# Kernel tuning notes

Measured on AMD Instinct MI355X. Metric: run time of the kernel, lower is better.

Reference implementation:

```python
import jax, jax.numpy as jnp
import numpy as np
import math

B, S = 8, 2048
N_HIDDEN_RNN = 512
D_MODEL = 1024
NUM_HEADS = 16
N_OUTPUT = 1024
SCALE = math.sqrt(D_MODEL // NUM_HEADS)  # head_dim used only for scaling


def setup_inputs() -> dict:
    key = jax.random.key(0)
    ks = jax.random.split(key, 11)
    def lin(k, fan_in, fan_out):
        bound = 1.0 / math.sqrt(fan_in)
        kw, kb = jax.random.split(k)
        W = jax.random.uniform(kw, (fan_out, fan_in), jnp.float32, -bound, bound)
        b = jax.random.uniform(kb, (fan_out,), jnp.float32, -bound, bound)
        return W, b
    Wq, bq = lin(ks[0], N_HIDDEN_RNN, D_MODEL)
    Wk, bk = lin(ks[1], D_MODEL, D_MODEL)
    Wv, bv = lin(ks[2], D_MODEL, D_MODEL)
    Wo, bo = lin(ks[3], D_MODEL, N_OUTPUT)
    return {
        "query": jax.random.normal(ks[4], (B, S, N_HIDDEN_RNN), jnp.float32),
        "key": jax.random.normal(ks[5], (B, S, D_MODEL), jnp.float32),
        "value": jax.random.normal(ks[6], (B, S, D_MODEL), jnp.float32),
        "Wq": Wq, "bq": bq, "Wk": Wk, "bk": bk,
        "Wv": Wv, "bv": bv, "Wo": Wo, "bo": bo,
    }


def reference(query, key, value, Wq, bq, Wk, bk, Wv, bv, Wo, bo):
    # Projections
    q = query @ Wq.T + bq      # [B, S, d_model]
    k = key @ Wk.T + bk        # [B, S, d_model]
    v = value @ Wv.T + bv      # [B, S, d_model]
    # Original code transposes to [B, d_model, S] (feature-axis attention).
    # scores[b, i, j] = sum_s q[b, s, i] * k[b, s, j] / scale -> [B, d, d]
    scores = jnp.einsum('bsi,bsj->bij', q, k) / SCALE
    probs = jax.nn.softmax(scores, axis=-1)   # softmax over feature axis j
    # out[b, s, i] = sum_j probs[b, i, j] * v[b, s, j]
    attn_out = jnp.einsum('bij,bsj->bsi', probs, v)  # [B, S, d_model]
    return attn_out @ Wo.T + bo  # [B, S, n_output]
```

## Files before the change

### kernel.cpp

```cpp
#include <hip/hip_runtime.h>
#include <hip/hip_bf16.h>
#include <stdint.h>

typedef __bf16 b16x8 __attribute__((ext_vector_type(8)));
typedef float  f32x4 __attribute__((ext_vector_type(4)));

__device__ __forceinline__ unsigned short f2bf(float f) {
    uint32_t u = __float_as_uint(f);
    u += 0x7fffu + ((u >> 16) & 1u);
    return (unsigned short)(u >> 16);
}
__device__ __forceinline__ float bf2f(unsigned short s) {
    return __uint_as_float(((uint32_t)s) << 16);
}

__device__ __forceinline__ void gld16(const unsigned short* g, unsigned short* l) {
    __builtin_amdgcn_global_load_lds(
        (const __attribute__((address_space(1))) void*)g,
        (__attribute__((address_space(3))) void*)l, 16, 0, 0);
}

__global__ void k_detect(const unsigned short* __restrict__ q, int n, int* __restrict__ flag) {
    float m = 0.f;
    for (int i = threadIdx.x; i < n; i += 256) {
        float f = fabsf(bf2f(q[i]));
        if (!(f < 1e30f)) f = 1e30f;
        m = fmaxf(m, f);
    }
#pragma unroll
    for (int o = 32; o > 0; o >>= 1) m = fmaxf(m, __shfl_xor(m, o));
    __shared__ float red[4];
    if ((threadIdx.x & 63) == 0) red[threadIdx.x >> 6] = m;
    __syncthreads();
    if (threadIdx.x == 0) {
        m = fmaxf(fmaxf(red[0], red[1]), fmaxf(red[2], red[3]));
        flag[0] = (m > 1e6f) ? 1 : 0;
    }
}

__global__ __launch_bounds__(256) void k_cvt(const void* __restrict__ src,
                                             unsigned short* __restrict__ dst,
                                             long n8, const int* __restrict__ flag) {
    long i = blockIdx.x * 256L + threadIdx.x;
    long stride = (long)gridDim.x * 256L;
    if (flag[0]) {
        const float4* s = (const float4*)src;
        for (long j = i; j < n8; j += stride) {
            float4 a = s[2 * j], b = s[2 * j + 1];
            uint4 o;
            o.x = f2bf(a.x) | ((uint32_t)f2bf(a.y) << 16);
            o.y = f2bf(a.z) | ((uint32_t)f2bf(a.w) << 16);
            o.z = f2bf(b.x) | ((uint32_t)f2bf(b.y) << 16);
            o.w = f2bf(b.z) | ((uint32_t)f2bf(b.w) << 16);
            ((uint4*)dst)[j] = o;
        }
    } else {
        const uint4* s = (const uint4*)src;
        for (long j = i; j < n8; j += stride) ((uint4*)dst)[j] = s[j];
    }
}

__global__ __launch_bounds__(256) void k_cvt_bias(const void* b0, const void* b1,
                                                  const void* b2, const void* b3,
                                                  float* __restrict__ dst,
                                                  const int* __restrict__ flag) {
    int i = blockIdx.x * 256 + threadIdx.x;
    int which = i >> 10, idx = i & 1023;
    const void* src = (which == 0) ? b0 : (which == 1) ? b1 : (which == 2) ? b2 : b3;
    dst[i] = flag[0] ? ((const float*)src)[idx] : bf2f(((const unsigned short*)src)[idx]);
}

template <int MODE>
__global__ __launch_bounds__(512, 2) void k_gemmA(
    const unsigned short* __restrict__ A, const unsigned short* __restrict__ B,
    const float* __restrict__ bias, void* __restrict__ Cv,
    int N, int K, int ldA, int ldB, int lb,
    long sAb, long sBb, long sCb, float scale,
    const int* __restrict__ flagp)
{
    extern __shared__ unsigned short lds_raw[];
    const int tid  = threadIdx.x;
    const int lane = tid & 63;
    const int wave = tid >> 6;
    const int nwg = gridDim.x * gridDim.y;
    const int bid = blockIdx.y * gridDim.x + blockIdx.x;
    const int vb  = (bid & 7) * (nwg >> 3) + (bid >> 3);
    const int bn  = (vb & (gridDim.x - 1)) * 256;
    const int bm  = (vb / gridDim.x) * 256;
    const int batch = bm >> lb;
    const int am0 = bm & ((1 << lb) - 1);
    const int Mb = 1 << lb;
    const unsigned short* Ab = A + (long)batch * sAb;
    const unsigned short* Bb = B + (long)batch * sBb;
    const long zC = (long)batch * sCb;
    const int wm = (wave >> 2) * 128;
    const int wn = (wave & 3) * 64;

    f32x4 acc[8][4];
    const f32x4 zero = {0.f, 0.f, 0.f, 0.f};
#pragma unroll
    for (int i = 0; i < 8; ++i)
#pragma unroll
        for (int j = 0; j < 4; ++j) acc[i][j] = zero;

    auto stage = [&](int kt, int cb) {
        unsigned short* LA = lds_raw + (size_t)cb * 32768;
        unsigned short* LB = LA + 16384;
#pragma unroll
        for (int j = 0; j < 4; ++j) {
            const int d = j * 512 + tid;
            const int row = d >> 3;
            const int klo = (d & 7) ^ (row & 7);
            gld16(Ab + (long)(am0 + row) * ldA + kt * 64 + klo * 8, LA + (size_t)d * 8);
            gld16(Bb + (long)(bn + row) * ldB + kt * 64 + klo * 8, LB + (size_t)d * 8);
        }
    };
    auto ctile = [&](int cb) {
        const unsigned short* LA = lds_raw + (size_t)cb * 32768;
        const unsigned short* LB = LA + 16384;
        b16x8 bfr[4][2];
#pragma unroll
        for (int p = 0; p < 4; ++p) {
            if (p == 0) {
#pragma unroll
                for (int j = 0; j < 4; ++j)
#pragma unroll
                    for (int s = 0; s < 2; ++s) {
                        const int r = wn + j * 16 + (lane & 15);
                        const int kl = s * 4 + (lane >> 4);
                        bfr[j][s] = *(const b16x8*)(LB + ((size_t)r * 8 + (kl ^ (r & 7))) * 8);
                    }
            }
            b16x8 a[2][2];
#pragma unroll
            for (int q = 0; q < 2; ++q)
#pragma unroll
                for (int s = 0; s < 2; ++s) {
                    const int r = wm + (2 * p + q) * 16 + (lane & 15);
                    const int kl = s * 4 + (lane >> 4);
                    a[q][s] = *(const b16x8*)(LA + ((size_t)r * 8 + (kl ^ (r & 7))) * 8);
                }
            __builtin_amdgcn_s_setprio(1);
#pragma unroll
            for (int q = 0; q < 2; ++q)
#pragma unroll
                for (int j = 0; j < 4; ++j)
#pragma unroll
                    for (int s = 0; s < 2; ++s)
                        acc[2 * p + q][j] = __builtin_amdgcn_mfma_f32_16x16x32_bf16(
                            a[q][s], bfr[j][s], acc[2 * p + q][j], 0, 0, 0);
            __builtin_amdgcn_s_setprio(0);
        }
    };

    const int NT = K >> 6;
    stage(0, 0);
    __syncthreads();
    int cur = 0;
    for (int kt = 0; kt < NT - 1; ++kt) {
        stage(kt + 1, cur ^ 1);
        ctile(cur);
        __syncthreads();
        cur ^= 1;
    }
    ctile(cur);

    const int fl = flagp ? flagp[0] : 1;
#pragma unroll
    for (int i = 0; i < 8; ++i)
#pragma unroll
        for (int j = 0; j < 4; ++j) {
            const int rloc = am0 + wm + i * 16 + (lane >> 4) * 4;
            const int n    = bn + wn + j * 16 + (lane & 15);
            const float bv = (MODE != 2 && bias != nullptr) ? bias[n] : 0.f;
            if (MODE == 0) {
                unsigned short* C = (unsigned short*)Cv;
#pragma unroll
                for (int r = 0; r < 4; ++r)
                    C[zC + (long)(rloc + r) * N + n] = f2bf(acc[i][j][r] * scale + bv);
            } else if (MODE == 1) {
                unsigned short* C = (unsigned short*)Cv;
                uint32_t p0 = f2bf(acc[i][j][0] * scale + bv) |
                              ((uint32_t)f2bf(acc[i][j][1] * scale + bv) << 16);
                uint32_t p1 = f2bf(acc[i][j][2] * scale + bv) |
                              ((uint32_t)f2bf(acc[i][j][3] * scale + bv) << 16);
                uint2 val; val.x = p0; val.y = p1;
                *(uint2*)(C + zC + (long)n * Mb + rloc) = val;
            } else if (MODE == 2) {
                float* C = (float*)Cv;
#pragma unroll
                for (int r = 0; r < 4; ++r)
                    C[zC + (long)(rloc + r) * N + n] = acc[i][j][r] * scale;
            } else {
                if (fl) {
                    float* C = (float*)Cv;
#pragma unroll
                    for (int r = 0; r < 4; ++r)
                        C[zC + (long)(rloc + r) * N + n] = acc[i][j][r] * scale + bv;
                } else {
                    unsigned short* C = (unsigned short*)Cv;
#pragma unroll
                    for (int r = 0; r < 4; ++r)
                        C[zC + (long)(rloc + r) * N + n] = f2bf(acc[i][j][r] * scale + bv);
                }
            }
        }
}

template <int MODE>
__global__ __launch_bounds__(512, 4) void k_gemmB(
    const unsigned short* __restrict__ A, const unsigned short* __restrict__ B,
    const float* __restrict__ bias, void* __restrict__ Cv,
    int N, int K, int ldA, int ldB, int lb,
    long sAb, long sBb, long sCb, float scale)
{
    extern __shared__ unsigned short lds_raw[];
    const int tid  = threadIdx.x;
    const int lane = tid & 63;
    const int wave = tid >> 6;
    const int nwg = gridDim.x * gridDim.y;
    const int bid = blockIdx.y * gridDim.x + blockIdx.x;
    const int vb  = (bid & 7) * (nwg >> 3) + (bid >> 3);
    const int bn  = (vb & (gridDim.x - 1)) * 256;
    const int bm  = (vb / gridDim.x) * 128;
    const int batch = bm >> lb;
    const int am0 = bm & ((1 << lb) - 1);
    const int Mb = 1 << lb;
    const unsigned short* Ab = A + (long)batch * sAb;
    const unsigned short* Bb = B + (long)batch * sBb;
    const long zC = (long)batch * sCb;
    const int wm = (wave >> 2) * 64;
    const int wn = (wave & 3) * 64;

    f32x4 acc[4][4];
    const f32x4 zero = {0.f, 0.f, 0.f, 0.f};
#pragma unroll
    for (int i = 0; i < 4; ++i)
#pragma unroll
        for (int j = 0; j < 4; ++j) acc[i][j] = zero;

    auto stage = [&](int kt, int cb) {
        unsigned short* Lb = lds_raw + (size_t)cb * 12288;
        {
            const int c = tid, row = c >> 2;
            const int klo = (c & 3) ^ ((row >> 1) & 3);
            gld16(Ab + (long)(am0 + row) * ldA + kt * 32 + klo * 8, Lb + (size_t)c * 8);
        }
#pragma unroll
        for (int j = 0; j < 2; ++j) {
            const int c = j * 512 + tid, row = c >> 2;
            const int klo = (c & 3) ^ ((row >> 1) & 3);
            gld16(Bb + (long)(bn + row) * ldB + kt * 32 + klo * 8, Lb + 4096 + (size_t)c * 8);
        }
    };
    auto ctile = [&](int cb) {
        const unsigned short* LA = lds_raw + (size_t)cb * 12288;
        const unsigned short* LB = LA + 4096;
        const int kl = lane >> 4;
        b16x8 af[4], bf[4];
#pragma unroll
        for (int j = 0; j < 4; ++j) {
            const int r = wn + j * 16 + (lane & 15);
            bf[j] = *(const b16x8*)(LB + ((size_t)r * 4 + (kl ^ ((r >> 1) & 3))) * 8);
        }
#pragma unroll
        for (int i = 0; i < 4; ++i) {
            const int r = wm + i * 16 + (lane & 15);
            af[i] = *(const b16x8*)(LA + ((size_t)r * 4 + (kl ^ ((r >> 1) & 3))) * 8);
        }
        __builtin_amdgcn_s_setprio(1);
#pragma unroll
        for (int i = 0; i < 4; ++i)
#pragma unroll
            for (int j = 0; j < 4; ++j)
                acc[i][j] = __builtin_amdgcn_mfma_f32_16x16x32_bf16(af[i], bf[j], acc[i][j], 0, 0, 0);
        __builtin_amdgcn_s_setprio(0);
    };

    const int NT = K >> 5;
    stage(0, 0);
    __syncthreads();
    int cur = 0;
    for (int kt = 0; kt < NT - 1; ++kt) {
        stage(kt + 1, cur ^ 1);
        ctile(cur);
        __syncthreads();
        cur ^= 1;
    }
    ctile(cur);

#pragma unroll
    for (int i = 0; i < 4; ++i)
#pragma unroll
        for (int j = 0; j < 4; ++j) {
            const int rloc = am0 + wm + i * 16 + (lane >> 4) * 4;
            const int n    = bn + wn + j * 16 + (lane & 15);
            const float bv = (MODE != 2 && bias != nullptr) ? bias[n] : 0.f;
            if (MODE == 0) {
                unsigned short* C = (unsigned short*)Cv;
#pragma unroll
                for (int r = 0; r < 4; ++r)
                    C[zC + (long)(rloc + r) * N + n] = f2bf(acc[i][j][r] * scale + bv);
            } else if (MODE == 1) {
                unsigned short* C = (unsigned short*)Cv;
                uint32_t p0 = f2bf(acc[i][j][0] * scale + bv) |
                              ((uint32_t)f2bf(acc[i][j][1] * scale + bv) << 16);
                uint32_t p1 = f2bf(acc[i][j][2] * scale + bv) |
                              ((uint32_t)f2bf(acc[i][j][3] * scale + bv) << 16);
                uint2 val; val.x = p0; val.y = p1;
                *(uint2*)(C + zC + (long)n * Mb + rloc) = val;
            } else {
                float* C = (float*)Cv;
#pragma unroll
                for (int r = 0; r < 4; ++r)
                    C[zC + (long)(rloc + r) * N + n] = acc[i][j][r] * scale;
            }
        }
}

template <int MODE>
__global__ __launch_bounds__(512, 2) void k_gemmC(
    const unsigned short* __restrict__ A, const unsigned short* __restrict__ B,
    const float* __restrict__ bias, void* __restrict__ Cv,
    int N, int K, int ldA, int ldB, int lb,
    long sAb, long sBb, long sCb, float scale)
{
    extern __shared__ unsigned short lds_raw[];
    const int tid  = threadIdx.x;
    const int lane = tid & 63;
    const int wave = tid >> 6;
    const int nwg = gridDim.x * gridDim.y;
    const int bid = blockIdx.y * gridDim.x + blockIdx.x;
    const int vb  = (bid & 7) * (nwg >> 3) + (bid >> 3);
    const int bn  = (vb & (gridDim.x - 1)) * 256;
    const int bm  = (vb / gridDim.x) * 256;
    const int batch = bm >> lb;
    const int am0 = bm & ((1 << lb) - 1);
    const unsigned short* Ab = A + (long)batch * sAb;
    const unsigned short* Bb = B + (long)batch * sBb;
    const long zC = (long)batch * sCb;
    const int g  = wave >> 2;
    const int wn = (wave & 3) * 64;

    f32x4 acc[8][4];
    const f32x4 zero = {0.f, 0.f, 0.f, 0.f};
#pragma unroll
    for (int i = 0; i < 8; ++i)
#pragma unroll
        for (int j = 0; j < 4; ++j) acc[i][j] = zero;

    auto stageQ = [&](int kt, int cb, int q) {
        unsigned short* Lbase = lds_raw + (size_t)cb * 32768 + ((q < 2) ? 16384 : 0);
#pragma unroll
        for (int j = 0; j < 2; ++j) {
            const int c = (q & 1) * 1024 + j * 512 + tid;
            const int row = c >> 3;
            const int klo = (c & 7) ^ (row & 7);
            if (q < 2)
                gld16(Bb + (long)(bn + row) * ldB + kt * 64 + klo * 8, Lbase + (size_t)c * 8);
            else
                gld16(Ab + (long)(am0 + row) * ldA + kt * 64 + klo * 8, Lbase + (size_t)c * 8);
        }
    };

    const int NT = K >> 6;
#pragma unroll
    for (int q = 0; q < 4; ++q) stageQ(0, 0, q);

    int cur = 0;
    for (int t = 0; t < NT; ++t) {
        const int has_next = (t + 1 < NT);
        const unsigned short* LA = lds_raw + (size_t)cur * 32768;
        const unsigned short* LB = LA + 16384;
        b16x8 bfr[4][2];
#pragma unroll
        for (int p = 0; p < 4; ++p) {
            if (p == 0) {
                asm volatile("s_waitcnt vmcnt(2)" ::: "memory");
            } else if (p == 2) {
                if (has_next) asm volatile("s_waitcnt vmcnt(4)" ::: "memory");
                else          asm volatile("s_waitcnt vmcnt(0)" ::: "memory");
            }
            __builtin_amdgcn_sched_barrier(0);
            __builtin_amdgcn_s_barrier();
            asm volatile("" ::: "memory");
            if (p == 0) {
#pragma unroll
                for (int j = 0; j < 4; ++j)
#pragma unroll
                    for (int s = 0; s < 2; ++s) {
                        const int r = wn + j * 16 + (lane & 15);
                        const int kl = s * 4 + (lane >> 4);
                        bfr[j][s] = *(const b16x8*)(LB + ((size_t)r * 8 + (kl ^ (r & 7))) * 8);
                    }
            }
            b16x8 afr[2][2];
#pragma unroll
            for (int r = 0; r < 2; ++r)
#pragma unroll
                for (int s = 0; s < 2; ++s) {
                    const int row = (p >> 1) * 128 + (p & 1) * 64 + g * 32 + r * 16 + (lane & 15);
                    const int kl = s * 4 + (lane >> 4);
                    afr[r][s] = *(const b16x8*)(LA + ((size_t)row * 8 + (kl ^ (row & 7))) * 8);
                }
            if (has_next) stageQ(t + 1, cur ^ 1, p);
            asm volatile("" ::: "memory");
            __builtin_amdgcn_s_barrier();
            __builtin_amdgcn_sched_barrier(0);
            __builtin_amdgcn_s_setprio(1);
#pragma unroll
            for (int r = 0; r < 2; ++r)
#pragma unroll
                for (int j = 0; j < 4; ++j)
#pragma unroll
                    for (int s = 0; s < 2; ++s)
                        acc[p * 2 + r][j] = __builtin_amdgcn_mfma_f32_16x16x32_bf16(
                            afr[r][s], bfr[j][s], acc[p * 2 + r][j], 0, 0, 0);
            __builtin_amdgcn_s_setprio(0);
        }
        cur ^= 1;
    }

#pragma unroll
    for (int i = 0; i < 8; ++i) {
        const int p = i >> 1, r = i & 1;
        const int rloc = am0 + (p >> 1) * 128 + (p & 1) * 64 + g * 32 + r * 16 + (lane >> 4) * 4;
#pragma unroll
        for (int j = 0; j < 4; ++j) {
            const int n = bn + wn + j * 16 + (lane & 15);
            const float bv = (bias != nullptr) ? bias[n] : 0.f;
            unsigned short* C = (unsigned short*)Cv;
#pragma unroll
            for (int rr = 0; rr < 4; ++rr)
                C[zC + (long)(rloc + rr) * N + n] = f2bf(acc[i][j][rr] * scale + bv);
        }
    }
}

__global__ __launch_bounds__(256) void k_softmax(float* __restrict__ S) {
    const long row = blockIdx.x;
    float* s = S + row * 1024;
    unsigned short* p = (unsigned short*)s;
    const int tid = threadIdx.x;
    float4 v = ((const float4*)s)[tid];
    float m = fmaxf(fmaxf(v.x, v.y), fmaxf(v.z, v.w));
#pragma unroll
    for (int o = 32; o > 0; o >>= 1) m = fmaxf(m, __shfl_xor(m, o));
    __shared__ float sm[4], ss[4];
    if ((tid & 63) == 0) sm[tid >> 6] = m;
    __syncthreads();
    m = fmaxf(fmaxf(sm[0], sm[1]), fmaxf(sm[2], sm[3]));
    float e0 = __expf(v.x - m), e1 = __expf(v.y - m);
    float e2 = __expf(v.z - m), e3 = __expf(v.w - m);
    float sum = e0 + e1 + e2 + e3;
#pragma unroll
    for (int o = 32; o > 0; o >>= 1) sum += __shfl_xor(sum, o);
    if ((tid & 63) == 0) ss[tid >> 6] = sum;
    __syncthreads();
    float inv = 1.f / (ss[0] + ss[1] + ss[2] + ss[3]);
    uint32_t w0 = f2bf(e0 * inv) | ((uint32_t)f2bf(e1 * inv) << 16);
    uint32_t w1 = f2bf(e2 * inv) | ((uint32_t)f2bf(e3 * inv) << 16);
    uint2 val; val.x = w0; val.y = w1;
    *(uint2*)(p + tid * 4) = val;
}

extern "C" void kernel_launch(void* const* d_in, const int* in_sizes, int n_in,
                              void* d_out, int out_size, void* d_ws, size_t ws_size,
                              hipStream_t stream) {
    (void)in_sizes; (void)n_in; (void)out_size; (void)ws_size;
    const void* q_in = d_in[0];
    const void* k_in = d_in[1];
    const void* v_in = d_in[2];
    const void* Wq   = d_in[3];
    const void* bq   = d_in[4];
    const void* Wk   = d_in[5];
    const void* bk   = d_in[6];
    const void* Wv   = d_in[7];
    const void* bv   = d_in[8];
    const void* Wo   = d_in[9];
    const void* bo   = d_in[10];

    const size_t MB = 1u << 20;
    const size_t LDS_A = 131072, LDS_B = 49152;
    hipFuncSetAttribute((const void*)k_gemmA<0>, hipFuncAttributeMaxDynamicSharedMemorySize, (int)LDS_A);
    hipFuncSetAttribute((const void*)k_gemmA<2>, hipFuncAttributeMaxDynamicSharedMemorySize, (int)LDS_A);
    hipFuncSetAttribute((const void*)k_gemmA<3>, hipFuncAttributeMaxDynamicSharedMemorySize, (int)LDS_A);
    hipFuncSetAttribute((const void*)k_gemmB<1>, hipFuncAttributeMaxDynamicSharedMemorySize, (int)LDS_B);
    hipFuncSetAttribute((const void*)k_gemmC<0>, hipFuncAttributeMaxDynamicSharedMemorySize, (int)LDS_A);

    char* ws = (char*)d_ws;
    int*            flag = (int*)ws;
    unsigned short* R1   = (unsigned short*)(ws + 1 * MB);
    unsigned short* R2   = (unsigned short*)(ws + 33 * MB);
    char*           R3   = ws + 65 * MB;
    unsigned short* kb = R1, *qb = R1, *vb = R1;
    unsigned short* Kt = R2, *attn = R2;
    float*          scores = (float*)R1;
    unsigned short* P      = R1;
    unsigned short* wqb = (unsigned short*)R3;
    unsigned short* wkb = (unsigned short*)(R3 + 1 * MB);
    unsigned short* wvb = (unsigned short*)(R3 + 3 * MB);
    unsigned short* wob = (unsigned short*)(R3 + 5 * MB);
    float*          bias4 = (float*)(R3 + 7 * MB);
    unsigned short* Vp = (unsigned short*)d_out;
    unsigned short* Qt = (unsigned short*)((char*)d_out + 32 * MB);

    dim3 blk(256), blk5(512);
    k_detect<<<1, blk, 0, stream>>>((const unsigned short*)q_in, 4096, flag);
    k_cvt_bias<<<16, blk, 0, stream>>>(bq, bk, bv, bo, bias4, flag);
    k_cvt<<<256, blk, 0, stream>>>(Wq, wqb, 1024L * 512 / 8, flag);
    k_cvt<<<512, blk, 0, stream>>>(Wk, wkb, 1024L * 1024 / 8, flag);
    k_cvt<<<512, blk, 0, stream>>>(Wv, wvb, 1024L * 1024 / 8, flag);
    k_cvt<<<512, blk, 0, stream>>>(Wo, wob, 1024L * 1024 / 8, flag);

    k_cvt<<<2048, blk, 0, stream>>>(k_in, kb, 8L * 2048 * 1024 / 8, flag);
    k_gemmB<1><<<dim3(4, 128), blk5, LDS_B, stream>>>(
        kb, wkb, bias4 + 1024, Kt, 1024, 1024, 1024, 1024, 11,
        2048L * 1024, 0, 1024L * 2048, 1.f);
    k_cvt<<<2048, blk, 0, stream>>>(q_in, qb, 8L * 2048 * 512 / 8, flag);
    k_gemmB<1><<<dim3(4, 128), blk5, LDS_B, stream>>>(
        qb, wqb, bias4, Qt, 1024, 512, 512, 512, 11,
        2048L * 512, 0, 1024L * 2048, 1.f);
    k_cvt<<<2048, blk, 0, stream>>>(v_in, vb, 8L * 2048 * 1024 / 8, flag);
    k_gemmA<0><<<dim3(4, 64), blk5, LDS_A, stream>>>(
        vb, wvb, bias4 + 2 * 1024, Vp, 1024, 1024, 1024, 1024, 24,
        0, 0, 0, 1.f, nullptr);
    k_gemmA<2><<<dim3(4, 32), blk5, LDS_A, stream>>>(
        Qt, Kt, nullptr, scores, 1024, 2048, 2048, 2048, 10,
        1024L * 2048, 1024L * 2048, 1024L * 1024, 0.125f, nullptr);
    k_softmax<<<dim3(8192), blk, 0, stream>>>(scores);
    k_gemmC<0><<<dim3(4, 64), blk5, LDS_A, stream>>>(
        Vp, P, nullptr, attn, 1024, 1024, 1024, 2048, 11,
        2048L * 1024, 1024L * 2048, 2048L * 1024, 1.f);
    k_gemmA<3><<<dim3(4, 64), blk5, LDS_A, stream>>>(
        attn, wob, bias4 + 3 * 1024, d_out, 1024, 1024, 1024, 1024, 24,
        0, 0, 0, 1.f, flag);
}
```

Measured before the change: 331.4 us.

## Add 4-stage pipelined GEMM kernel with K=32 tiles and route four GEMMs through it

Adds a new GEMM kernel, k_gemmD, that prefetches three K=32 tiles ahead into a four-deep LDS ring buffer. Its vmcnt waits are hand-tuned and it uses one barrier pair per step. It replaces the double-buffered K=64 kernels for the K projection, the V projection, the P·V product and the output projection, and drops the earlier gemmC kernel. The aim is deeper overlap of global-to-LDS loads with MFMA work. The cost is more barriers per K step, a narrower swizzle that may cause LDS bank conflicts, and 256x256 tiles for the K projection where it previously used a smaller-LDS kernel at higher occupancy.

```diff
diff --git a/kernel.cpp b/kernel.cpp
--- a/kernel.cpp
+++ b/kernel.cpp
@@ -71,7 +71,7 @@
 }
 
 template <int MODE>
-__global__ __launch_bounds__(512, 2) void k_gemmA(
+__global__ __launch_bounds__(512) void k_gemmD(
     const unsigned short* __restrict__ A, const unsigned short* __restrict__ B,
     const float* __restrict__ bias, void* __restrict__ Cv,
     int N, int K, int ldA, int ldB, int lb,
@@ -93,7 +93,7 @@
     const unsigned short* Ab = A + (long)batch * sAb;
     const unsigned short* Bb = B + (long)batch * sBb;
     const long zC = (long)batch * sCb;
-    const int wm = (wave >> 2) * 128;
+    const int g  = wave >> 2;
     const int wn = (wave & 3) * 64;
 
     f32x4 acc[8][4];
@@ -103,76 +103,62 @@
 #pragma unroll
         for (int j = 0; j < 4; ++j) acc[i][j] = zero;
 
-    auto stage = [&](int kt, int cb) {
-        unsigned short* LA = lds_raw + (size_t)cb * 32768;
-        unsigned short* LB = LA + 16384;
-#pragma unroll
-        for (int j = 0; j < 4; ++j) {
-            const int d = j * 512 + tid;
-            const int row = d >> 3;
-            const int klo = (d & 7) ^ (row & 7);
-            gld16(Ab + (long)(am0 + row) * ldA + kt * 64 + klo * 8, LA + (size_t)d * 8);
-            gld16(Bb + (long)(bn + row) * ldB + kt * 64 + klo * 8, LB + (size_t)d * 8);
+    auto stageD = [&](int t) {
+        unsigned short* S = lds_raw + (size_t)(t & 3) * 16384;
+#pragma unroll
+        for (int j = 0; j < 2; ++j) {
+            const int c = j * 512 + tid;
+            const int row = c >> 2;
+            const int klo = (c & 3) ^ ((row >> 1) & 3);
+            gld16(Ab + (long)(am0 + row) * ldA + t * 32 + klo * 8, S + (size_t)c * 8);
+            gld16(Bb + (long)(bn + row) * ldB + t * 32 + klo * 8, S + 8192 + (size_t)c * 8);
         }
     };
-    auto ctile = [&](int cb) {
-        const unsigned short* LA = lds_raw + (size_t)cb * 32768;
-        const unsigned short* LB = LA + 16384;
-        b16x8 bfr[4][2];
-#pragma unroll
-        for (int p = 0; p < 4; ++p) {
-            if (p == 0) {
-#pragma unroll
-                for (int j = 0; j < 4; ++j)
-#pragma unroll
-                    for (int s = 0; s < 2; ++s) {
-                        const int r = wn + j * 16 + (lane & 15);
-                        const int kl = s * 4 + (lane >> 4);
-                        bfr[j][s] = *(const b16x8*)(LB + ((size_t)r * 8 + (kl ^ (r & 7))) * 8);
-                    }
-            }
-            b16x8 a[2][2];
-#pragma unroll
-            for (int q = 0; q < 2; ++q)
-#pragma unroll
-                for (int s = 0; s < 2; ++s) {
-                    const int r = wm + (2 * p + q) * 16 + (lane & 15);
-                    const int kl = s * 4 + (lane >> 4);
-                    a[q][s] = *(const b16x8*)(LA + ((size_t)r * 8 + (kl ^ (r & 7))) * 8);
-                }
-            __builtin_amdgcn_s_setprio(1);
-#pragma unroll
-            for (int q = 0; q < 2; ++q)
-#pragma unroll
-                for (int j = 0; j < 4; ++j)
-#pragma unroll
-                    for (int s = 0; s < 2; ++s)
-                        acc[2 * p + q][j] = __builtin_amdgcn_mfma_f32_16x16x32_bf16(
-                            a[q][s], bfr[j][s], acc[2 * p + q][j], 0, 0, 0);
-            __builtin_amdgcn_s_setprio(0);
-        }
-    };
-
-    const int NT = K >> 6;
-    stage(0, 0);
-    __syncthreads();
-    int cur = 0;
-    for (int kt = 0; kt < NT - 1; ++kt) {
-        stage(kt + 1, cur ^ 1);
-        ctile(cur);
-        __syncthreads();
-        cur ^= 1;
-    }
-    ctile(cur);
+
+    const int NT = K >> 5;
+    stageD(0); stageD(1); stageD(2);
+
+    const int kl = lane >> 4;
+    for (int t = 0; t < NT; ++t) {
+        if (t + 3 < NT) stageD(t + 3);
+        if (t + 3 < NT)      asm volatile("s_waitcnt vmcnt(12)" ::: "memory");
+        else if (t + 2 < NT) asm volatile("s_waitcnt vmcnt(8)"  ::: "memory");
+        else if (t + 1 < NT) asm volatile("s_waitcnt vmcnt(4)"  ::: "memory");
+        else                 asm volatile("s_waitcnt vmcnt(0)"  ::: "memory");
+        __builtin_amdgcn_s_barrier();
+        __builtin_amdgcn_sched_barrier(0);
+        const unsigned short* SA = lds_raw + (size_t)(t & 3) * 16384;
+        const unsigned short* SB = SA + 8192;
+        b16x8 af[8], bf[4];
+#pragma unroll
+        for (int j = 0; j < 4; ++j) {
+            const int r = wn + j * 16 + (lane & 15);
+            bf[j] = *(const b16x8*)(SB + ((size_t)r * 4 + (kl ^ ((r >> 1) & 3))) * 8);
+        }
+#pragma unroll
+        for (int i = 0; i < 8; ++i) {
+            const int r = g * 128 + i * 16 + (lane & 15);
+            af[i] = *(const b16x8*)(SA + ((size_t)r * 4 + (kl ^ ((r >> 1) & 3))) * 8);
+        }
+        __builtin_amdgcn_s_setprio(1);
+#pragma unroll
+        for (int i = 0; i < 8; ++i)
+#pragma unroll
+            for (int j = 0; j < 4; ++j)
+                acc[i][j] = __builtin_amdgcn_mfma_f32_16x16x32_bf16(af[i], bf[j], acc[i][j], 0, 0, 0);
+        __builtin_amdgcn_s_setprio(0);
+        __builtin_amdgcn_s_barrier();
+        __builtin_amdgcn_sched_barrier(0);
+    }
 
     const int fl = flagp ? flagp[0] : 1;
 #pragma unroll
     for (int i = 0; i < 8; ++i)
 #pragma unroll
         for (int j = 0; j < 4; ++j) {
-            const int rloc = am0 + wm + i * 16 + (lane >> 4) * 4;
+            const int rloc = am0 + g * 128 + i * 16 + (lane >> 4) * 4;
             const int n    = bn + wn + j * 16 + (lane & 15);
-            const float bv = (MODE != 2 && bias != nullptr) ? bias[n] : 0.f;
+            const float bv = (bias != nullptr) ? bias[n] : 0.f;
             if (MODE == 0) {
                 unsigned short* C = (unsigned short*)Cv;
 #pragma unroll
@@ -186,11 +172,6 @@
                               ((uint32_t)f2bf(acc[i][j][3] * scale + bv) << 16);
                 uint2 val; val.x = p0; val.y = p1;
                 *(uint2*)(C + zC + (long)n * Mb + rloc) = val;
-            } else if (MODE == 2) {
-                float* C = (float*)Cv;
-#pragma unroll
-                for (int r = 0; r < 4; ++r)
-                    C[zC + (long)(rloc + r) * N + n] = acc[i][j][r] * scale;
             } else {
                 if (fl) {
                     float* C = (float*)Cv;
@@ -207,8 +188,112 @@
         }
 }
 
-template <int MODE>
-__global__ __launch_bounds__(512, 4) void k_gemmB(
+__global__ __launch_bounds__(512, 2) void k_gemmA2(
+    const unsigned short* __restrict__ A, const unsigned short* __restrict__ B,
+    void* __restrict__ Cv,
+    int N, int K, int ldA, int ldB, int lb,
+    long sAb, long sBb, long sCb, float scale)
+{
+    extern __shared__ unsigned short lds_raw[];
+    const int tid  = threadIdx.x;
+    const int lane = tid & 63;
+    const int wave = tid >> 6;
+    const int nwg = gridDim.x * gridDim.y;
+    const int bid = blockIdx.y * gridDim.x + blockIdx.x;
+    const int vb  = (bid & 7) * (nwg >> 3) + (bid >> 3);
+    const int bn  = (vb & (gridDim.x - 1)) * 256;
+    const int bm  = (vb / gridDim.x) * 256;
+    const int batch = bm >> lb;
+    const int am0 = bm & ((1 << lb) - 1);
+    const unsigned short* Ab = A + (long)batch * sAb;
+    const unsigned short* Bb = B + (long)batch * sBb;
+    const long zC = (long)batch * sCb;
+    const int wm = (wave >> 2) * 128;
+    const int wn = (wave & 3) * 64;
+
+    f32x4 acc[8][4];
+    const f32x4 zero = {0.f, 0.f, 0.f, 0.f};
+#pragma unroll
+    for (int i = 0; i < 8; ++i)
+#pragma unroll
+        for (int j = 0; j < 4; ++j) acc[i][j] = zero;
+
+    auto stage = [&](int kt, int cb) {
+        unsigned short* LA = lds_raw + (size_t)cb * 32768;
+        unsigned short* LB = LA + 16384;
+#pragma unroll
+        for (int j = 0; j < 4; ++j) {
+            const int d = j * 512 + tid;
+            const int row = d >> 3;
+            const int klo = (d & 7) ^ (row & 7);
+            gld16(Ab + (long)(am0 + row) * ldA + kt * 64 + klo * 8, LA + (size_t)d * 8);
+            gld16(Bb + (long)(bn + row) * ldB + kt * 64 + klo * 8, LB + (size_t)d * 8);
+        }
+    };
+    auto ctile = [&](int cb) {
+        const unsigned short* LA = lds_raw + (size_t)cb * 32768;
+        const unsigned short* LB = LA + 16384;
+        b16x8 bfr[4][2];
+#pragma unroll
+        for (int p = 0; p < 4; ++p) {
+            if (p == 0) {
+#pragma unroll
+                for (int j = 0; j < 4; ++j)
+#pragma unroll
+                    for (int s = 0; s < 2; ++s) {
+                        const int r = wn + j * 16 + (lane & 15);
+                        const int klq = s * 4 + (lane >> 4);
+                        bfr[j][s] = *(const b16x8*)(LB + ((size_t)r * 8 + (klq ^ (r & 7))) * 8);
+                    }
+            }
+            b16x8 a[2][2];
+#pragma unroll
+            for (int q = 0; q < 2; ++q)
+#pragma unroll
+                for (int s = 0; s < 2; ++s) {
+                    const int r = wm + (2 * p + q) * 16 + (lane & 15);
+                    const int klq = s * 4 + (lane >> 4);
+                    a[q][s] = *(const b16x8*)(LA + ((size_t)r * 8 + (klq ^ (r & 7))) * 8);
+                }
+            __builtin_amdgcn_s_setprio(1);
+#pragma unroll
+            for (int q = 0; q < 2; ++q)
+#pragma unroll
+                for (int j = 0; j < 4; ++j)
+#pragma unroll
+                    for (int s = 0; s < 2; ++s)
+                        acc[2 * p + q][j] = __builtin_amdgcn_mfma_f32_16x16x32_bf16(
+                            a[q][s], bfr[j][s], acc[2 * p + q][j], 0, 0, 0);
+            __builtin_amdgcn_s_setprio(0);
+        }
+    };
+
+    const int NT = K >> 6;
+    stage(0, 0);
+    __syncthreads();
+    int cur = 0;
+    for (int kt = 0; kt < NT - 1; ++kt) {
+        stage(kt + 1, cur ^ 1);
+        ctile(cur);
+        __syncthreads();
+        cur ^= 1;
+    }
+    ctile(cur);
+
+#pragma unroll
+    for (int i = 0; i < 8; ++i)
+#pragma unroll
+        for (int j = 0; j < 4; ++j) {
+            const int rloc = am0 + wm + i * 16 + (lane >> 4) * 4;
+            const int n    = bn + wn + j * 16 + (lane & 15);
+            float* C = (float*)Cv;
+#pragma unroll
+            for (int r = 0; r < 4; ++r)
+                C[zC + (long)(rloc + r) * N + n] = acc[i][j][r] * scale;
+        }
+}
+
+__global__ __launch_bounds__(512, 4) void k_gemmB1(
     const unsigned short* __restrict__ A, const unsigned short* __restrict__ B,
     const float* __restrict__ bias, void* __restrict__ Cv,
     int N, int K, int ldA, int ldB, int lb,
@@ -295,146 +380,15 @@
         for (int j = 0; j < 4; ++j) {
             const int rloc = am0 + wm + i * 16 + (lane >> 4) * 4;
             const int n    = bn + wn + j * 16 + (lane & 15);
-            const float bv = (MODE != 2 && bias != nullptr) ? bias[n] : 0.f;
-            if (MODE == 0) {
-                unsigned short* C = (unsigned short*)Cv;
-#pragma unroll
-                for (int r = 0; r < 4; ++r)
-                    C[zC + (long)(rloc + r) * N + n] = f2bf(acc[i][j][r] * scale + bv);
-            } else if (MODE == 1) {
-                unsigned short* C = (unsigned short*)Cv;
-                uint32_t p0 = f2bf(acc[i][j][0] * scale + bv) |
-                              ((uint32_t)f2bf(acc[i][j][1] * scale + bv) << 16);
-                uint32_t p1 = f2bf(acc[i][j][2] * scale + bv) |
-                              ((uint32_t)f2bf(acc[i][j][3] * scale + bv) << 16);
-                uint2 val; val.x = p0; val.y = p1;
-                *(uint2*)(C + zC + (long)n * Mb + rloc) = val;
-            } else {
-                float* C = (float*)Cv;
-#pragma unroll
-                for (int r = 0; r < 4; ++r)
-                    C[zC + (long)(rloc + r) * N + n] = acc[i][j][r] * scale;
-            }
-        }
-}
-
-template <int MODE>
-__global__ __launch_bounds__(512, 2) void k_gemmC(
-    const unsigned short* __restrict__ A, const unsigned short* __restrict__ B,
-    const float* __restrict__ bias, void* __restrict__ Cv,
-    int N, int K, int ldA, int ldB, int lb,
-    long sAb, long sBb, long sCb, float scale)
-{
-    extern __shared__ unsigned short lds_raw[];
-    const int tid  = threadIdx.x;
-    const int lane = tid & 63;
-    const int wave = tid >> 6;
-    const int nwg = gridDim.x * gridDim.y;
-    const int bid = blockIdx.y * gridDim.x + blockIdx.x;
-    const int vb  = (bid & 7) * (nwg >> 3) + (bid >> 3);
-    const int bn  = (vb & (gridDim.x - 1)) * 256;
-    const int bm  = (vb / gridDim.x) * 256;
-    const int batch = bm >> lb;
-    const int am0 = bm & ((1 << lb) - 1);
-    const unsigned short* Ab = A + (long)batch * sAb;
-    const unsigned short* Bb = B + (long)batch * sBb;
-    const long zC = (long)batch * sCb;
-    const int g  = wave >> 2;
-    const int wn = (wave & 3) * 64;
-
-    f32x4 acc[8][4];
-    const f32x4 zero = {0.f, 0.f, 0.f, 0.f};
-#pragma unroll
-    for (int i = 0; i < 8; ++i)
-#pragma unroll
-        for (int j = 0; j < 4; ++j) acc[i][j] = zero;
-
-    auto stageQ = [&](int kt, int cb, int q) {
-        unsigned short* Lbase = lds_raw + (size_t)cb * 32768 + ((q < 2) ? 16384 : 0);
-#pragma unroll
-        for (int j = 0; j < 2; ++j) {
-            const int c = (q & 1) * 1024 + j * 512 + tid;
-            const int row = c >> 3;
-            const int klo = (c & 7) ^ (row & 7);
-            if (q < 2)
-                gld16(Bb + (long)(bn + row) * ldB + kt * 64 + klo * 8, Lbase + (size_t)c * 8);
-            else
-                gld16(Ab + (long)(am0 + row) * ldA + kt * 64 + klo * 8, Lbase + (size_t)c * 8);
-        }
-    };
-
-    const int NT = K >> 6;
-#pragma unroll
-    for (int q = 0; q < 4; ++q) stageQ(0, 0, q);
-
-    int cur = 0;
-    for (int t = 0; t < NT; ++t) {
-        const int has_next = (t + 1 < NT);
-        const unsigned short* LA = lds_raw + (size_t)cur * 32768;
-        const unsigned short* LB = LA + 16384;
-        b16x8 bfr[4][2];
-#pragma unroll
-        for (int p = 0; p < 4; ++p) {
-            if (p == 0) {
-                asm volatile("s_waitcnt vmcnt(2)" ::: "memory");
-            } else if (p == 2) {
-                if (has_next) asm volatile("s_waitcnt vmcnt(4)" ::: "memory");
-                else          asm volatile("s_waitcnt vmcnt(0)" ::: "memory");
-            }
-            __builtin_amdgcn_sched_barrier(0);
-            __builtin_amdgcn_s_barrier();
-            asm volatile("" ::: "memory");
-            if (p == 0) {
-#pragma unroll
-                for (int j = 0; j < 4; ++j)
-#pragma unroll
-                    for (int s = 0; s < 2; ++s) {
-                        const int r = wn + j * 16 + (lane & 15);
-                        const int kl = s * 4 + (lane >> 4);
-                        bfr[j][s] = *(const b16x8*)(LB + ((size_t)r * 8 + (kl ^ (r & 7))) * 8);
-                    }
-            }
-            b16x8 afr[2][2];
-#pragma unroll
-            for (int r = 0; r < 2; ++r)
-#pragma unroll
-                for (int s = 0; s < 2; ++s) {
-                    const int row = (p >> 1) * 128 + (p & 1) * 64 + g * 32 + r * 16 + (lane & 15);
-                    const int kl = s * 4 + (lane >> 4);
-                    afr[r][s] = *(const b16x8*)(LA + ((size_t)row * 8 + (kl ^ (row & 7))) * 8);
-                }
-            if (has_next) stageQ(t + 1, cur ^ 1, p);
-            asm volatile("" ::: "memory");
-            __builtin_amdgcn_s_barrier();
-            __builtin_amdgcn_sched_barrier(0);
-            __builtin_amdgcn_s_setprio(1);
-#pragma unroll
-            for (int r = 0; r < 2; ++r)
-#pragma unroll
-                for (int j = 0; j < 4; ++j)
-#pragma unroll
-                    for (int s = 0; s < 2; ++s)
-                        acc[p * 2 + r][j] = __builtin_amdgcn_mfma_f32_16x16x32_bf16(
-                            afr[r][s], bfr[j][s], acc[p * 2 + r][j], 0, 0, 0);
-            __builtin_amdgcn_s_setprio(0);
-        }
-        cur ^= 1;
-    }
-
-#pragma unroll
-    for (int i = 0; i < 8; ++i) {
-        const int p = i >> 1, r = i & 1;
-        const int rloc = am0 + (p >> 1) * 128 + (p & 1) * 64 + g * 32 + r * 16 + (lane >> 4) * 4;
-#pragma unroll
-        for (int j = 0; j < 4; ++j) {
-            const int n = bn + wn + j * 16 + (lane & 15);
             const float bv = (bias != nullptr) ? bias[n] : 0.f;
             unsigned short* C = (unsigned short*)Cv;
-#pragma unroll
-            for (int rr = 0; rr < 4; ++rr)
-                C[zC + (long)(rloc + rr) * N + n] = f2bf(acc[i][j][rr] * scale + bv);
-        }
-    }
+            uint32_t p0 = f2bf(acc[i][j][0] * scale + bv) |
+                          ((uint32_t)f2bf(acc[i][j][1] * scale + bv) << 16);
+            uint32_t p1 = f2bf(acc[i][j][2] * scale + bv) |
+                          ((uint32_t)f2bf(acc[i][j][3] * scale + bv) << 16);
+            uint2 val; val.x = p0; val.y = p1;
+            *(uint2*)(C + zC + (long)n * Mb + rloc) = val;
+        }
 }
 
 __global__ __launch_bounds__(256) void k_softmax(float* __restrict__ S) {
@@ -481,12 +435,12 @@
     const void* bo   = d_in[10];
 
     const size_t MB = 1u << 20;
-    const size_t LDS_A = 131072, LDS_B = 49152;
-    hipFuncSetAttribute((const void*)k_gemmA<0>, hipFuncAttributeMaxDynamicSharedMemorySize, (int)LDS_A);
-    hipFuncSetAttribute((const void*)k_gemmA<2>, hipFuncAttributeMaxDynamicSharedMemorySize, (int)LDS_A);
-    hipFuncSetAttribute((const void*)k_gemmA<3>, hipFuncAttributeMaxDynamicSharedMemorySize, (int)LDS_A);
-    hipFuncSetAttribute((const void*)k_gemmB<1>, hipFuncAttributeMaxDynamicSharedMemorySize, (int)LDS_B);
-    hipFuncSetAttribute((const void*)k_gemmC<0>, hipFuncAttributeMaxDynamicSharedMemorySize, (int)LDS_A);
+    const size_t LDS_D = 131072, LDS_A = 131072, LDS_B = 49152;
+    hipFuncSetAttribute((const void*)k_gemmD<0>, hipFuncAttributeMaxDynamicSharedMemorySize, (int)LDS_D);
+    hipFuncSetAttribute((const void*)k_gemmD<1>, hipFuncAttributeMaxDynamicSharedMemorySize, (int)LDS_D);
+    hipFuncSetAttribute((const void*)k_gemmD<3>, hipFuncAttributeMaxDynamicSharedMemorySize, (int)LDS_D);
+    hipFuncSetAttribute((const void*)k_gemmA2,   hipFuncAttributeMaxDynamicSharedMemorySize, (int)LDS_A);
+    hipFuncSetAttribute((const void*)k_gemmB1,   hipFuncAttributeMaxDynamicSharedMemorySize, (int)LDS_B);
 
     char* ws = (char*)d_ws;
     int*            flag = (int*)ws;
@@ -514,25 +468,25 @@
     k_cvt<<<512, blk, 0, stream>>>(Wo, wob, 1024L * 1024 / 8, flag);
 
     k_cvt<<<2048, blk, 0, stream>>>(k_in, kb, 8L * 2048 * 1024 / 8, flag);
-    k_gemmB<1><<<dim3(4, 128), blk5, LDS_B, stream>>>(
+    k_gemmD<1><<<dim3(4, 64), blk5, LDS_D, stream>>>(
         kb, wkb, bias4 + 1024, Kt, 1024, 1024, 1024, 1024, 11,
-        2048L * 1024, 0, 1024L * 2048, 1.f);
+        2048L * 1024, 0, 1024L * 2048, 1.f, nullptr);
     k_cvt<<<2048, blk, 0, stream>>>(q_in, qb, 8L * 2048 * 512 / 8, flag);
-    k_gemmB<1><<<dim3(4, 128), blk5, LDS_B, stream>>>(
+    k_gemmB1<<<dim3(4, 128), blk5, LDS_B, stream>>>(
         qb, wqb, bias4, Qt, 1024, 512, 512, 512, 11,
         2048L * 512, 0, 1024L * 2048, 1.f);
     k_cvt<<<2048, blk, 0, stream>>>(v_in, vb, 8L * 2048 * 1024 / 8, flag);
-    k_gemmA<0><<<dim3(4, 64), blk5, LDS_A, stream>>>(
+    k_gemmD<0><<<dim3(4, 64), blk5, LDS_D, stream>>>(
         vb, wvb, bias4 + 2 * 1024, Vp, 1024, 1024, 1024, 1024, 24,
         0, 0, 0, 1.f, nullptr);
-    k_gemmA<2><<<dim3(4, 32), blk5, LDS_A, stream>>>(
-        Qt, Kt, nullptr, scores, 1024, 2048, 2048, 2048, 10,
-        1024L * 2048, 1024L * 2048, 1024L * 1024, 0.125f, nullptr);
+    k_gemmA2<<<dim3(4, 32), blk5, LDS_A, stream>>>(
+        Qt, Kt, scores, 1024, 2048, 2048, 2048, 10,
+        1024L * 2048, 1024L * 2048, 1024L * 1024, 0.125f);
     k_softmax<<<dim3(8192), blk, 0, stream>>>(scores);
-    k_gemmC<0><<<dim3(4, 64), blk5, LDS_A, stream>>>(
+    k_gemmD<0><<<dim3(4, 64), blk5, LDS_D, stream>>>(
         Vp, P, nullptr, attn, 1024, 1024, 1024, 2048, 11,
-        2048L * 1024, 1024L * 2048, 2048L * 1024, 1.f);
-    k_gemmA<3><<<dim3(4, 64), blk5, LDS_A, stream>>>(
+        2048L * 1024, 1024L * 2048, 2048L * 1024, 1.f, nullptr);
+    k_gemmD<3><<<dim3(4, 64), blk5, LDS_D, stream>>>(
         attn, wob, bias4 + 3 * 1024, d_out, 1024, 1024, 1024, 1024, 24,
         0, 0, 0, 1.f, flag);
 }
```

After: 334.7 us. About the same (+1.0%).
